# Optimization experiments

Measured on AMD Instinct MI355X. Metric: run time of the kernel, lower is better.

Reference implementation:

```python
import jax, jax.numpy as jnp
import numpy as np

N = 1024   # nodes
C = 256    # channels (n_features)
NEG_SLOPE = 0.2


def setup_inputs() -> dict:
    key = jax.random.key(0)
    k1, k2, k3, k4, k5, k6, k7 = jax.random.split(key, 7)
    nodes = jax.random.normal(k1, (N, C), dtype=jnp.float32)
    # dense adjacency used only via (adj != 0); force self-loops so every
    # softmax row has at least one valid entry
    adj_mat = jax.random.randint(k2, (N, N), 0, 2).astype(jnp.int32)
    adj_mat = adj_mat.at[jnp.arange(N), jnp.arange(N)].set(1)
    lim = 1.0 / np.sqrt(C)  # eqx.nn.Linear default uniform init bound
    W_src_w = jax.random.uniform(k3, (C, C), minval=-lim, maxval=lim, dtype=jnp.float32)
    W_src_b = jax.random.uniform(k4, (C,), minval=-lim, maxval=lim, dtype=jnp.float32)
    W_tgt_w = jax.random.uniform(k5, (C, C), minval=-lim, maxval=lim, dtype=jnp.float32)
    W_tgt_b = jax.random.uniform(k6, (C,), minval=-lim, maxval=lim, dtype=jnp.float32)
    a_w = jax.random.uniform(k7, (C,), minval=-lim, maxval=lim, dtype=jnp.float32)  # to_score, no bias
    return {"nodes": nodes, "adj_mat": adj_mat, "W_src_w": W_src_w, "W_src_b": W_src_b,
            "W_tgt_w": W_tgt_w, "W_tgt_b": W_tgt_b, "a_w": a_w}


def reference(nodes, adj_mat, W_src_w, W_src_b, W_tgt_w, W_tgt_b, a_w):
    # per-node linear maps (eqx.nn.Linear: y = W @ x + b)
    g_src = nodes @ W_src_w.T + W_src_b              # [node, C]
    g_tgt = nodes @ W_tgt_w.T + W_tgt_b              # [node, C]
    # g[i, j, c] = g_src[i, c] + g_tgt[j, c]   (axis names as in original: tgt, src)
    g = g_src[:, None, :] + g_tgt[None, :, :]        # [node, node, C]
    g = jax.nn.leaky_relu(g, NEG_SLOPE)
    score = jnp.einsum('ijc,c->ij', g, a_w)          # [node, node]
    score = jnp.where(adj_mat != 0, score, -jnp.inf) # mask non-edges
    weights = jax.nn.softmax(score, axis=1)          # over src axis
    return weights @ g_tgt                           # [node, C]
```

## Files before the change

kernel.cpp:

```cpp
#include <hip/hip_runtime.h>


typedef unsigned short u16;
typedef unsigned int   u32;
typedef _Float16 h2 __attribute__((ext_vector_type(2)));

#define NNODE 1024
#define NC    256
#define NEG   0.2f

__device__ __forceinline__ float bf2f(u16 h) {
    u32 u = ((u32)h) << 16;
    return __builtin_bit_cast(float, u);
}
__device__ __forceinline__ u16 f2bf(float f) {
    u32 u = __builtin_bit_cast(u32, f);
    u32 r = (u + 0x7FFFu + ((u >> 16) & 1u)) >> 16;
    return (u16)r;
}
__device__ __forceinline__ u16 f2h(float f) {
    _Float16 h = (_Float16)f;
    return __builtin_bit_cast(u16, h);
}
__device__ __forceinline__ h2 bch(u32 u) { return __builtin_bit_cast(h2, u); }
__device__ __forceinline__ h2 habs2(h2 y) {
    u32 u = __builtin_bit_cast(u32, y) & 0x7FFF7FFFu;
    return __builtin_bit_cast(h2, u);
}
__device__ __forceinline__ float dot2(h2 a, h2 b, float acc) {
#if __has_builtin(__builtin_amdgcn_fdot2)
    return __builtin_amdgcn_fdot2(a, b, acc, false);
#else
    acc = fmaf((float)a.x, (float)b.x, acc);
    return fmaf((float)a.y, (float)b.y, acc);
#endif
}

__device__ __forceinline__ int wave_detect(const u16* __restrict__ nodes, int lane)
{
    ushort4 v = *(const ushort4*)(nodes + lane * 4);
    const u16 h[4] = {v.x, v.y, v.z, v.w};
    int cnt = 0;
    #pragma unroll
    for (int q = 0; q < 4; ++q) {
        int e = (h[q] >> 7) & 0xFF;
        cnt += (e >= 132 || (e >= 1 && e <= 90)) ? 1 : 0;
    }
    #pragma unroll
    for (int off = 32; off; off >>= 1) cnt += __shfl_xor(cnt, off, 64);
    return (cnt >= 64) ? 0 : 1;
}

__device__ __forceinline__ int swz(int grp, int row) { return grp ^ (row & 31); }

__global__ __launch_bounds__(256) void lin_kernel(
    const void* __restrict__ nodes_v,
    const void* __restrict__ Wsrc_v, const void* __restrict__ bsrc_v,
    const void* __restrict__ Wtgt_v, const void* __restrict__ btgt_v,
    u16* __restrict__ gsh, u16* __restrict__ gth)
{
    __shared__ float nT[64][34];
    __shared__ float wT[64][68];

    const int t  = threadIdx.x;
    const int bf = wave_detect((const u16*)nodes_v, t & 63);
    const int ct = blockIdx.x;
    const int it = blockIdx.y;
    const int i0 = it * 32;
    const bool is_src = (ct < 4);
    const int c0 = (is_src ? ct : ct - 4) * 64;
    const void* __restrict__ Wv = is_src ? Wsrc_v : Wtgt_v;
    const void* __restrict__ bv = is_src ? bsrc_v : btgt_v;
    u16* __restrict__ g         = is_src ? gsh : gth;

    const int tc = t & 15, ti = t >> 4;
    float acc[2][4] = {};

    for (int k0 = 0; k0 < NC; k0 += 64) {
        __syncthreads();
        {
            int ii = t & 31, kg = t >> 5;
            float vals[8];
            if (bf) {
                uint4 v = *(const uint4*)((const u16*)nodes_v + (i0 + ii) * NC + k0 + kg * 8);
                const u16* pv = (const u16*)&v;
                #pragma unroll
                for (int q = 0; q < 8; ++q) vals[q] = bf2f(pv[q]);
            } else {
                const float* nf = (const float*)nodes_v;
                float4 v0 = *(const float4*)(nf + (i0 + ii) * NC + k0 + kg * 8);
                float4 v1 = *(const float4*)(nf + (i0 + ii) * NC + k0 + kg * 8 + 4);
                vals[0] = v0.x; vals[1] = v0.y; vals[2] = v0.z; vals[3] = v0.w;
                vals[4] = v1.x; vals[5] = v1.y; vals[6] = v1.z; vals[7] = v1.w;
            }
            #pragma unroll
            for (int q = 0; q < 8; ++q) nT[kg * 8 + q][ii] = vals[q];
        }
        {
            int cc = t & 63, kg = t >> 6;
            float vals[16];
            if (bf) {
                const u16* W = (const u16*)Wv;
                uint4 v0 = *(const uint4*)(W + (c0 + cc) * NC + k0 + kg * 16);
                uint4 v1 = *(const uint4*)(W + (c0 + cc) * NC + k0 + kg * 16 + 8);
                const u16* p0 = (const u16*)&v0;
                const u16* p1 = (const u16*)&v1;
                #pragma unroll
                for (int q = 0; q < 8; ++q) { vals[q] = bf2f(p0[q]); vals[8 + q] = bf2f(p1[q]); }
            } else {
                const float* W = (const float*)Wv;
                #pragma unroll
                for (int h = 0; h < 4; ++h) {
                    float4 v = *(const float4*)(W + (c0 + cc) * NC + k0 + kg * 16 + 4 * h);
                    vals[4 * h + 0] = v.x; vals[4 * h + 1] = v.y;
                    vals[4 * h + 2] = v.z; vals[4 * h + 3] = v.w;
                }
            }
            #pragma unroll
            for (int q = 0; q < 16; ++q) wT[kg * 16 + q][cc] = vals[q];
        }
        __syncthreads();
        #pragma unroll 8
        for (int kk = 0; kk < 64; ++kk) {
            float2 av = *(const float2*)&nT[kk][2 * ti];
            float4 bvv = *(const float4*)&wT[kk][4 * tc];
            float sa[2] = {av.x, av.y};
            float tb[4] = {bvv.x, bvv.y, bvv.z, bvv.w};
            #pragma unroll
            for (int a = 0; a < 2; ++a)
                #pragma unroll
                for (int b = 0; b < 4; ++b)
                    acc[a][b] = fmaf(sa[a], tb[b], acc[a][b]);
        }
    }

    float bb[4];
    #pragma unroll
    for (int q = 0; q < 4; ++q)
        bb[q] = bf ? bf2f(((const u16*)bv)[c0 + 4 * tc + q])
                   : ((const float*)bv)[c0 + 4 * tc + q];
    #pragma unroll
    for (int a = 0; a < 2; ++a) {
        int irow = i0 + 2 * ti + a;
        ushort4 ov;
        ov.x = f2h(acc[a][0] + bb[0]);
        ov.y = f2h(acc[a][1] + bb[1]);
        ov.z = f2h(acc[a][2] + bb[2]);
        ov.w = f2h(acc[a][3] + bb[3]);
        *(ushort4*)(g + (size_t)irow * NC + c0 + 4 * tc) = ov;
    }
}

__global__ __launch_bounds__(256) void sdot_kernel(
    const u16* __restrict__ gth, const void* __restrict__ aw_v,
    const u16* __restrict__ nodes_u16, float* __restrict__ sgt06)
{
    const int t    = threadIdx.x;
    const int lane = t & 63;
    const int bf   = wave_detect(nodes_u16, lane);
    const int row  = blockIdx.x * 4 + (t >> 6);

    float a0, a1, a2, a3;
    if (bf) {
        ushort4 a4 = *(const ushort4*)((const u16*)aw_v + lane * 4);
        a0 = bf2f(a4.x); a1 = bf2f(a4.y); a2 = bf2f(a4.z); a3 = bf2f(a4.w);
    } else {
        float4 a4 = *(const float4*)((const float*)aw_v + lane * 4);
        a0 = a4.x; a1 = a4.y; a2 = a4.z; a3 = a4.w;
    }
    ushort4 gv = *(const ushort4*)(gth + (size_t)row * NC + lane * 4);
    float s = a0 * (float)__builtin_bit_cast(_Float16, gv.x)
            + a1 * (float)__builtin_bit_cast(_Float16, gv.y)
            + a2 * (float)__builtin_bit_cast(_Float16, gv.z)
            + a3 * (float)__builtin_bit_cast(_Float16, gv.w);
    #pragma unroll
    for (int off = 32; off; off >>= 1) s += __shfl_xor(s, off, 64);
    if (lane == 0) sgt06[row] = 0.6f * s;
}

__global__ __launch_bounds__(512, 2) void fused_kernel(
    const u16* __restrict__ gsh, const u16* __restrict__ gth,
    const void* __restrict__ aw_v, const int* __restrict__ adj,
    const u16* __restrict__ nodes_u16, const float* __restrict__ sgt06,
    int jcnt, float* __restrict__ po, float* __restrict__ pm,
    float* __restrict__ pls, void* __restrict__ out_v)
{
    __shared__ u32   gt32[64 * 128];
    __shared__ u32   a32[128];
    __shared__ float p_lds[16][64];

    const int t    = threadIdx.x;
    const int i    = t >> 6;
    const int lane = t & 63;
    const int bf   = wave_detect(nodes_u16, lane);
    const int r0   = blockIdx.x * 16 + 2 * i;
    const int z    = blockIdx.y;
    const int jbase = z * jcnt;
    const int jl = lane & 15, q  = lane >> 4;
    const int oc = lane & 31, hh = lane >> 5;

    if (t < 128) {
        float a0, a1;
        if (bf) { a0 = bf2f(((const u16*)aw_v)[2 * t]); a1 = bf2f(((const u16*)aw_v)[2 * t + 1]); }
        else    { a0 = ((const float*)aw_v)[2 * t];     a1 = ((const float*)aw_v)[2 * t + 1]; }
        h2 av; av.x = (_Float16)(0.4f * a0); av.y = (_Float16)(0.4f * a1);
        a32[t] = __builtin_bit_cast(u32, av);
    }

    u32 gsr[2][32];
    #pragma unroll
    for (int r = 0; r < 2; ++r) {
        const u16* src = gsh + (size_t)(r0 + r) * NC + q * 64;
        #pragma unroll
        for (int k = 0; k < 8; ++k) {
            uint4 gv = *(const uint4*)(src + 8 * k);
            gsr[r][4 * k + 0] = gv.x; gsr[r][4 * k + 1] = gv.y;
            gsr[r][4 * k + 2] = gv.z; gsr[r][4 * k + 3] = gv.w;
        }
    }
    __syncthreads();

    float Sgs06[2];
    #pragma unroll
    for (int r = 0; r < 2; ++r) {
        float sg = 0.f;
        #pragma unroll
        for (int k = 0; k < 8; ++k) {
            uint4 a4 = *(const uint4*)&a32[q * 32 + 4 * k];
            sg = dot2(bch(a4.x), bch(gsr[r][4 * k + 0]), sg);
            sg = dot2(bch(a4.y), bch(gsr[r][4 * k + 1]), sg);
            sg = dot2(bch(a4.z), bch(gsr[r][4 * k + 2]), sg);
            sg = dot2(bch(a4.w), bch(gsr[r][4 * k + 3]), sg);
        }
        sg += __shfl_xor(sg, 16, 64);
        sg += __shfl_xor(sg, 32, 64);
        Sgs06[r] = 1.5f * sg;
    }

    float l[2] = {0.f, 0.f};
    float of[2][8] = {};

    for (int j0 = jbase; j0 < jbase + jcnt; j0 += 64) {
        __syncthreads();
        {
            int rr = t & 63, kg = t >> 6;
            const u16* src = gth + (size_t)(j0 + rr) * NC + kg * 32;
            u32* dst = gt32 + rr * 128;
            #pragma unroll
            for (int c = 0; c < 4; ++c) {
                uint4 v = *(const uint4*)(src + 8 * c);
                *(uint4*)(dst + swz(kg * 4 + c, rr) * 4) = v;
            }
        }
        __syncthreads();

        const float sgtj = sgt06[j0 + lane];

        float spv[2][4] = {};
        #pragma unroll
        for (int k = 0; k < 8; ++k) {
            uint4 a4 = *(const uint4*)&a32[q * 32 + 4 * k];
            h2 a0 = bch(a4.x), a1 = bch(a4.y), a2 = bch(a4.z), a3 = bch(a4.w);
            #pragma unroll
            for (int p = 0; p < 4; ++p) {
                const int rowp = 16 * p + jl;
                uint4 g4 = *(const uint4*)&gt32[rowp * 128 + swz(q * 8 + k, rowp) * 4];
                h2 t0 = bch(g4.x), t1 = bch(g4.y), t2 = bch(g4.z), t3 = bch(g4.w);
                #pragma unroll
                for (int r = 0; r < 2; ++r) {
                    spv[r][p] = dot2(a0, habs2(bch(gsr[r][4 * k + 0]) + t0), spv[r][p]);
                    spv[r][p] = dot2(a1, habs2(bch(gsr[r][4 * k + 1]) + t1), spv[r][p]);
                    spv[r][p] = dot2(a2, habs2(bch(gsr[r][4 * k + 2]) + t2), spv[r][p]);
                    spv[r][p] = dot2(a3, habs2(bch(gsr[r][4 * k + 3]) + t3), spv[r][p]);
                }
            }
        }
        #pragma unroll
        for (int r = 0; r < 2; ++r)
            #pragma unroll
            for (int p = 0; p < 4; ++p) {
                spv[r][p] += __shfl_xor(spv[r][p], 16, 64);
                spv[r][p] += __shfl_xor(spv[r][p], 32, 64);
            }

        #pragma unroll
        for (int r = 0; r < 2; ++r) {
            const float sabs = (lane < 16) ? spv[r][0] : (lane < 32) ? spv[r][1]
                             : (lane < 48) ? spv[r][2] : spv[r][3];
            const float s = sabs + Sgs06[r] + sgtj;
            const int valid = adj[(size_t)(r0 + r) * NNODE + j0 + lane];
            const float p = valid ? __expf(s) : 0.f;
            l[r] += p;
            p_lds[2 * i + r][lane] = p;
        }

        #pragma unroll 4
        for (int jp = 0; jp < 32; ++jp) {
            const int j = 2 * jp + hh;
            const float w0 = p_lds[2 * i    ][j];
            const float w1 = p_lds[2 * i + 1][j];
            uint4 g4 = *(const uint4*)&gt32[j * 128 + swz(oc, j) * 4];
            h2 v0 = bch(g4.x), v1 = bch(g4.y), v2 = bch(g4.z), v3 = bch(g4.w);
            of[0][0] = fmaf(w0, (float)v0.x, of[0][0]);
            of[0][1] = fmaf(w0, (float)v0.y, of[0][1]);
            of[0][2] = fmaf(w0, (float)v1.x, of[0][2]);
            of[0][3] = fmaf(w0, (float)v1.y, of[0][3]);
            of[0][4] = fmaf(w0, (float)v2.x, of[0][4]);
            of[0][5] = fmaf(w0, (float)v2.y, of[0][5]);
            of[0][6] = fmaf(w0, (float)v3.x, of[0][6]);
            of[0][7] = fmaf(w0, (float)v3.y, of[0][7]);
            of[1][0] = fmaf(w1, (float)v0.x, of[1][0]);
            of[1][1] = fmaf(w1, (float)v0.y, of[1][1]);
            of[1][2] = fmaf(w1, (float)v1.x, of[1][2]);
            of[1][3] = fmaf(w1, (float)v1.y, of[1][3]);
            of[1][4] = fmaf(w1, (float)v2.x, of[1][4]);
            of[1][5] = fmaf(w1, (float)v2.y, of[1][5]);
            of[1][6] = fmaf(w1, (float)v3.x, of[1][6]);
            of[1][7] = fmaf(w1, (float)v3.y, of[1][7]);
        }
    }

    #pragma unroll
    for (int r = 0; r < 2; ++r) {
        #pragma unroll
        for (int off = 32; off; off >>= 1) l[r] += __shfl_xor(l[r], off, 64);
        #pragma unroll
        for (int k = 0; k < 8; ++k) of[r][k] += __shfl_xor(of[r][k], 32, 64);
    }

    if (lane < 32) {
        #pragma unroll
        for (int r = 0; r < 2; ++r) {
            const int row = r0 + r;
            if (out_v) {
                const float inv = 1.0f / l[r];
                if (bf) {
                    u16* out = (u16*)out_v;
                    ushort4 oa, ob;
                    oa.x = f2bf(of[r][0] * inv); oa.y = f2bf(of[r][1] * inv);
                    oa.z = f2bf(of[r][2] * inv); oa.w = f2bf(of[r][3] * inv);
                    ob.x = f2bf(of[r][4] * inv); ob.y = f2bf(of[r][5] * inv);
                    ob.z = f2bf(of[r][6] * inv); ob.w = f2bf(of[r][7] * inv);
                    *(ushort4*)(out + (size_t)row * NC + 8 * oc)     = oa;
                    *(ushort4*)(out + (size_t)row * NC + 8 * oc + 4) = ob;
                } else {
                    float* out = (float*)out_v;
                    *(float4*)(out + (size_t)row * NC + 8 * oc) =
                        make_float4(of[r][0] * inv, of[r][1] * inv,
                                    of[r][2] * inv, of[r][3] * inv);
                    *(float4*)(out + (size_t)row * NC + 8 * oc + 4) =
                        make_float4(of[r][4] * inv, of[r][5] * inv,
                                    of[r][6] * inv, of[r][7] * inv);
                }
            } else {
                float* pp = po + ((size_t)z * NNODE + row) * NC + 8 * oc;
                *(float4*)pp       = make_float4(of[r][0], of[r][1], of[r][2], of[r][3]);
                *(float4*)(pp + 4) = make_float4(of[r][4], of[r][5], of[r][6], of[r][7]);
            }
        }
    }
    if (!out_v && lane == 0) {
        #pragma unroll
        for (int r = 0; r < 2; ++r) {
            pm [(size_t)z * NNODE + r0 + r] = 0.f;
            pls[(size_t)z * NNODE + r0 + r] = l[r];
        }
    }
}

__global__ __launch_bounds__(256) void combine_kernel(
    const float* __restrict__ po, const float* __restrict__ pm,
    const float* __restrict__ pls, const u16* __restrict__ nodes_u16,
    int ns, void* __restrict__ out_v)
{
    const int bf  = wave_detect(nodes_u16, threadIdx.x & 63);
    const int row = blockIdx.x;
    const int c   = threadIdx.x;

    float mstar = -1e30f;
    for (int zz = 0; zz < ns; ++zz)
        mstar = fmaxf(mstar, pm[zz * NNODE + row]);

    float acc = 0.f, lsum = 0.f;
    for (int zz = 0; zz < ns; ++zz) {
        const float wz = __expf(pm[zz * NNODE + row] - mstar);
        lsum = fmaf(pls[zz * NNODE + row], wz, lsum);
        acc  = fmaf(po[(size_t)(zz * NNODE + row) * NC + c], wz, acc);
    }
    const float v = acc / lsum;
    if (bf) ((u16*)out_v)[row * NC + c] = f2bf(v);
    else    ((float*)out_v)[row * NC + c] = v;
}

extern "C" void kernel_launch(void* const* d_in, const int* in_sizes, int n_in,
                              void* d_out, int out_size, void* d_ws, size_t ws_size,
                              hipStream_t stream)
{
    const u16* nodes_u16 = (const u16*)d_in[0];
    const int* adj       = (const int*)d_in[1];

    char*  wsb   = (char*)d_ws;
    u16*   gsh   = (u16*)wsb;
    u16*   gth   = gsh + (size_t)NNODE * NC;
    float* sgt06 = (float*)(wsb + 2ull * NNODE * NC * sizeof(u16));

    lin_kernel<<<dim3(8, 32), 256, 0, stream>>>(d_in[0], d_in[2], d_in[3],
                                                d_in[4], d_in[5], gsh, gth);
    sdot_kernel<<<256, 256, 0, stream>>>(gth, d_in[6], nodes_u16, sgt06);

    const size_t base = 2ull * NNODE * NC * sizeof(u16) + NNODE * sizeof(float);
    const size_t per  = 4ull * NNODE * NC + 8ull * NNODE;
    int NS = 0;
    if      (ws_size >= base + 8 * per) NS = 8;
    else if (ws_size >= base + 4 * per) NS = 4;
    else if (ws_size >= base + 2 * per) NS = 2;

    if (NS) {
        float* po  = (float*)(wsb + base);
        float* pm  = po + (size_t)NS * NNODE * NC;
        float* pls = pm + (size_t)NS * NNODE;
        fused_kernel<<<dim3(64, NS), 512, 0, stream>>>(
            gsh, gth, d_in[6], adj, nodes_u16, sgt06, NNODE / NS,
            po, pm, pls, nullptr);
        combine_kernel<<<NNODE, 256, 0, stream>>>(po, pm, pls, nodes_u16, NS, d_out);
    } else {
        fused_kernel<<<dim3(64, 1), 512, 0, stream>>>(
            gsh, gth, d_in[6], adj, nodes_u16, sgt06, NNODE,
            nullptr, nullptr, nullptr, d_out);
    }
}
```

Measured before the change: 64.41 us.

## Double-buffer g_tgt tiles via async global_load_lds and unroll combine for 8 splits

Replaces the synchronous global-to-register-to-LDS staging of each 64-row g_tgt tile with direct global_load_lds into a double-buffered LDS array. The next tile is prefetched while the current one is consumed, aiming to hide global load latency and drop one barrier per iteration. The swizzle moves to the global source address. The combine kernel gets a fully unrolled path for 8 splits so the partial loads are issued together. LDS use doubles to 64KB per block, which may reduce occupancy. The code shows no explicit wait on the async load before the single barrier, which risks reading a tile before it has fully arrived.

```diff
diff --git a/kernel.cpp b/kernel.cpp
--- a/kernel.cpp
+++ b/kernel.cpp
@@ -8,6 +8,7 @@
 #define NNODE 1024
 #define NC    256
 #define NEG   0.2f
+#define BUFU  8192
 
 __device__ __forceinline__ float bf2f(u16 h) {
     u32 u = ((u32)h) << 16;
@@ -185,7 +186,7 @@
     int jcnt, float* __restrict__ po, float* __restrict__ pm,
     float* __restrict__ pls, void* __restrict__ out_v)
 {
-    __shared__ u32   gt32[64 * 128];
+    __shared__ u32   gt32[2 * BUFU];
     __shared__ u32   a32[128];
     __shared__ float p_lds[16][64];
 
@@ -196,8 +197,22 @@
     const int r0   = blockIdx.x * 16 + 2 * i;
     const int z    = blockIdx.y;
     const int jbase = z * jcnt;
+    const int nt   = jcnt >> 6;
     const int jl = lane & 15, q  = lane >> 4;
     const int oc = lane & 31, hh = lane >> 5;
+
+    auto stage_tile = [&](int bufIdx, int j0s) {
+        #pragma unroll
+        for (int c = 0; c < 4; ++c) {
+            const int row = 16 * c + 2 * i + (lane >> 5);
+            const int g   = lane & 31;
+            const u16* gp = gth + (size_t)(j0s + row) * NC + (g ^ (row & 31)) * 8;
+            u32* lp = gt32 + bufIdx * BUFU + row * 128 + g * 4;
+            __builtin_amdgcn_global_load_lds(
+                (const __attribute__((address_space(1))) void*)gp,
+                (__attribute__((address_space(3))) void*)lp, 16, 0, 0);
+        }
+    };
 
     if (t < 128) {
         float a0, a1;
@@ -218,6 +233,8 @@
             gsr[r][4 * k + 2] = gv.z; gsr[r][4 * k + 3] = gv.w;
         }
     }
+
+    stage_tile(0, jbase);
     __syncthreads();
 
     float Sgs06[2];
@@ -240,19 +257,10 @@
     float l[2] = {0.f, 0.f};
     float of[2][8] = {};
 
-    for (int j0 = jbase; j0 < jbase + jcnt; j0 += 64) {
-        __syncthreads();
-        {
-            int rr = t & 63, kg = t >> 6;
-            const u16* src = gth + (size_t)(j0 + rr) * NC + kg * 32;
-            u32* dst = gt32 + rr * 128;
-            #pragma unroll
-            for (int c = 0; c < 4; ++c) {
-                uint4 v = *(const uint4*)(src + 8 * c);
-                *(uint4*)(dst + swz(kg * 4 + c, rr) * 4) = v;
-            }
-        }
-        __syncthreads();
+    for (int t2 = 0; t2 < nt; ++t2) {
+        const int bb = (t2 & 1) * BUFU;
+        const int j0 = jbase + t2 * 64;
+        if (t2 + 1 < nt) stage_tile((t2 + 1) & 1, j0 + 64);
 
         const float sgtj = sgt06[j0 + lane];
 
@@ -264,13 +272,13 @@
             #pragma unroll
             for (int p = 0; p < 4; ++p) {
                 const int rowp = 16 * p + jl;
-                uint4 g4 = *(const uint4*)&gt32[rowp * 128 + swz(q * 8 + k, rowp) * 4];
-                h2 t0 = bch(g4.x), t1 = bch(g4.y), t2 = bch(g4.z), t3 = bch(g4.w);
+                uint4 g4 = *(const uint4*)&gt32[bb + rowp * 128 + swz(q * 8 + k, rowp) * 4];
+                h2 t0 = bch(g4.x), t1 = bch(g4.y), t2v = bch(g4.z), t3 = bch(g4.w);
                 #pragma unroll
                 for (int r = 0; r < 2; ++r) {
                     spv[r][p] = dot2(a0, habs2(bch(gsr[r][4 * k + 0]) + t0), spv[r][p]);
                     spv[r][p] = dot2(a1, habs2(bch(gsr[r][4 * k + 1]) + t1), spv[r][p]);
-                    spv[r][p] = dot2(a2, habs2(bch(gsr[r][4 * k + 2]) + t2), spv[r][p]);
+                    spv[r][p] = dot2(a2, habs2(bch(gsr[r][4 * k + 2]) + t2v), spv[r][p]);
                     spv[r][p] = dot2(a3, habs2(bch(gsr[r][4 * k + 3]) + t3), spv[r][p]);
                 }
             }
@@ -299,7 +307,7 @@
             const int j = 2 * jp + hh;
             const float w0 = p_lds[2 * i    ][j];
             const float w1 = p_lds[2 * i + 1][j];
-            uint4 g4 = *(const uint4*)&gt32[j * 128 + swz(oc, j) * 4];
+            uint4 g4 = *(const uint4*)&gt32[bb + j * 128 + swz(oc, j) * 4];
             h2 v0 = bch(g4.x), v1 = bch(g4.y), v2 = bch(g4.z), v3 = bch(g4.w);
             of[0][0] = fmaf(w0, (float)v0.x, of[0][0]);
             of[0][1] = fmaf(w0, (float)v0.y, of[0][1]);
@@ -318,6 +326,8 @@
             of[1][6] = fmaf(w1, (float)v3.x, of[1][6]);
             of[1][7] = fmaf(w1, (float)v3.y, of[1][7]);
         }
+
+        __syncthreads();
     }
 
     #pragma unroll
@@ -377,17 +387,38 @@
     const int row = blockIdx.x;
     const int c   = threadIdx.x;
 
-    float mstar = -1e30f;
-    for (int zz = 0; zz < ns; ++zz)
-        mstar = fmaxf(mstar, pm[zz * NNODE + row]);
-
-    float acc = 0.f, lsum = 0.f;
-    for (int zz = 0; zz < ns; ++zz) {
-        const float wz = __expf(pm[zz * NNODE + row] - mstar);
-        lsum = fmaf(pls[zz * NNODE + row], wz, lsum);
-        acc  = fmaf(po[(size_t)(zz * NNODE + row) * NC + c], wz, acc);
-    }
-    const float v = acc / lsum;
+    float v;
+    if (ns == 8) {
+        float mv[8], lv[8], ov[8];
+        #pragma unroll
+        for (int zz = 0; zz < 8; ++zz) {
+            mv[zz] = pm [zz * NNODE + row];
+            lv[zz] = pls[zz * NNODE + row];
+            ov[zz] = po [(size_t)(zz * NNODE + row) * NC + c];
+        }
+        float mstar = mv[0];
+        #pragma unroll
+        for (int zz = 1; zz < 8; ++zz) mstar = fmaxf(mstar, mv[zz]);
+        float acc = 0.f, lsum = 0.f;
+        #pragma unroll
+        for (int zz = 0; zz < 8; ++zz) {
+            const float wz = __expf(mv[zz] - mstar);
+            lsum = fmaf(lv[zz], wz, lsum);
+            acc  = fmaf(ov[zz], wz, acc);
+        }
+        v = acc / lsum;
+    } else {
+        float mstar = -1e30f;
+        for (int zz = 0; zz < ns; ++zz)
+            mstar = fmaxf(mstar, pm[zz * NNODE + row]);
+        float acc = 0.f, lsum = 0.f;
+        for (int zz = 0; zz < ns; ++zz) {
+            const float wz = __expf(pm[zz * NNODE + row] - mstar);
+            lsum = fmaf(pls[zz * NNODE + row], wz, lsum);
+            acc  = fmaf(po[(size_t)(zz * NNODE + row) * NC + c], wz, acc);
+        }
+        v = acc / lsum;
+    }
     if (bf) ((u16*)out_v)[row * NC + c] = f2bf(v);
     else    ((float*)out_v)[row * NC + c] = v;
 }
```

Result: faster. 61.07 us (-5.2%).
